# Performance work log

Measured on AMD Instinct MI355X. Metric: run time of the kernel, lower is better.

Reference implementation:

```python
import jax, jax.numpy as jnp
import numpy as np

B, T, E, H, D = 2, 2048, 1024, 16, 64   # batch, seq, n_embd, heads, head_dim
C, P, BF, MH, R, F4 = 64, 64, 256, 128, 8, 4096  # ctx_dim, prototypes, basis, mod hidden, gate rank, 4*n_embd


def _rms(x):
    return x * jax.lax.rsqrt(jnp.mean(x * x, axis=-1, keepdims=True) + 1e-6)


def _rotary(x, cos, sin):
    d = x.shape[-1] // 2
    x1, x2 = x[..., :d], x[..., d:]
    return jnp.concatenate([x1 * cos + x2 * sin, -x1 * sin + x2 * cos], axis=-1)


def _ln(x, g, b):
    mu = jnp.mean(x, axis=-1, keepdims=True)
    v = jnp.mean(jnp.square(x - mu), axis=-1, keepdims=True)
    return (x - mu) * jax.lax.rsqrt(v + 1e-5) * g + b


def _remixed(x, ctx, bw, lg, lb, tm, bias, m1w, m1b, m2w, m2b, ogw, ogb, ogB, ogs):
    # RemixedLinear: basis proj -> LayerNorm -> context sigmoid gate -> template mixing -> low-rank output gate
    h = _ln(x @ bw.T, lg, lb)                                              # [B,T,basis]
    gl = jax.nn.gelu(ctx @ m1w.T + m1b, approximate=False) @ m2w.T + m2b   # basis_modulator MLP
    gate_basis = jax.nn.sigmoid(gl)                                        # gate_temperature = 1.0, dense gate
    gate_out = 1.0 + jnp.tanh(ogs * ((ctx @ ogw.T + ogb) @ ogB))           # low-rank output gate
    return (h * gate_basis) @ tm.T * gate_out + bias


def _forward(x, cos, sin, wq, wk, wv, wo, cb_qw, protos,
             fc_bw, fc_lg, fc_lb, fc_tm, fc_b, fc_m1w, fc_m1b, fc_m2w, fc_m2b, fc_ogw, fc_ogb, fc_ogB, fc_ogs,
             pj_bw, pj_lg, pj_lb, pj_tm, pj_b, pj_m1w, pj_m1b, pj_m2w, pj_m2b, pj_ogw, pj_ogb, pj_ogB, pj_ogs):
    b, t, _ = x.shape
    # --- attention with rotary embeddings ---
    xn = _rms(x)
    q = _rotary((xn @ wq.T).reshape(b, t, H, D), cos, sin)
    k = _rotary((xn @ wk.T).reshape(b, t, H, D), cos, sin)
    v = (xn @ wv.T).reshape(b, t, H, D)
    s = jnp.einsum('bqhd,bkhd->bhqk', q, k) * (D ** -0.5)
    mask = jnp.tril(jnp.ones((t, t), dtype=bool))
    s = jnp.where(mask, s, jnp.finfo(s.dtype).min)
    a = jax.nn.softmax(s, axis=-1)
    attn_out = jnp.einsum('bhqk,bkhd->bqhd', a, v).reshape(b, t, E) @ wo.T
    x = x + attn_out
    # --- ContextBank: soft lookup into prototype vocabulary ---
    xn2 = _rms(x)
    cq = xn2 @ cb_qw.T                                  # [B,T,C]
    w = jax.nn.softmax((cq @ protos.T) * (C ** -0.5), axis=-1)
    ctx = w @ protos                                    # [B,T,C]
    # --- RemixedFeedForward: RemixedLinear -> relu^2 -> RemixedLinear ---
    h = _remixed(xn2, ctx, fc_bw, fc_lg, fc_lb, fc_tm, fc_b, fc_m1w, fc_m1b, fc_m2w, fc_m2b, fc_ogw, fc_ogb, fc_ogB, fc_ogs)
    h = jnp.square(jax.nn.relu(h))
    y = _remixed(h, ctx, pj_bw, pj_lg, pj_lb, pj_tm, pj_b, pj_m1w, pj_m1b, pj_m2w, pj_m2b, pj_ogw, pj_ogb, pj_ogB, pj_ogs)
    return x + y


def setup_inputs():
    key = jax.random.key(0)
    ks = jax.random.split(key, 24)
    g = lambda i, shape, s=0.02: jax.random.normal(ks[i], shape, jnp.float32) * s
    t = jnp.arange(T, dtype=jnp.float32)
    inv = 1.0 / (10000.0 ** (jnp.arange(0, D, 2, dtype=jnp.float32) / D))
    ang = t[:, None] * inv                              # [T, D/2]
    return dict(
        x=jax.random.normal(ks[0], (B, T, E), jnp.float32),
        cos=jnp.cos(ang)[None, :, None, :], sin=jnp.sin(ang)[None, :, None, :],
        wq=g(1, (E, E)), wk=g(2, (E, E)), wv=g(3, (E, E)), wo=g(4, (E, E)),
        cb_qw=g(5, (C, E)), protos=g(6, (P, C)),
        fc_bw=g(7, (BF, E)), fc_lg=jnp.ones((BF,)), fc_lb=jnp.zeros((BF,)),
        fc_tm=g(8, (F4, BF), 0.05), fc_b=jnp.zeros((F4,)),
        fc_m1w=g(9, (MH, C)), fc_m1b=jnp.zeros((MH,)),
        fc_m2w=g(10, (BF, MH)), fc_m2b=jnp.zeros((BF,)),
        fc_ogw=g(11, (R, C)), fc_ogb=jnp.zeros((R,)),
        fc_ogB=g(12, (R, F4)), fc_ogs=jnp.full((1,), 0.1, jnp.float32),
        pj_bw=g(13, (BF, F4)), pj_lg=jnp.ones((BF,)), pj_lb=jnp.zeros((BF,)),
        pj_tm=g(14, (E, BF), 0.05), pj_b=jnp.zeros((E,)),
        pj_m1w=g(15, (MH, C)), pj_m1b=jnp.zeros((MH,)),
        pj_m2w=g(16, (BF, MH)), pj_m2b=jnp.zeros((BF,)),
        pj_ogw=g(17, (R, C)), pj_ogb=jnp.zeros((R,)),
        pj_ogB=g(18, (R, E)), pj_ogs=jnp.full((1,), 0.1, jnp.float32),
    )


def reference(x, cos, sin, wq, wk, wv, wo, cb_qw, protos,
              fc_bw, fc_lg, fc_lb, fc_tm, fc_b, fc_m1w, fc_m1b, fc_m2w, fc_m2b, fc_ogw, fc_ogb, fc_ogB, fc_ogs,
              pj_bw, pj_lg, pj_lb, pj_tm, pj_b, pj_m1w, pj_m1b, pj_m2w, pj_m2b, pj_ogw, pj_ogb, pj_ogB, pj_ogs):
    return _forward(x, cos, sin, wq, wk, wv, wo, cb_qw, protos,
                    fc_bw, fc_lg, fc_lb, fc_tm, fc_b, fc_m1w, fc_m1b, fc_m2w, fc_m2b, fc_ogw, fc_ogb, fc_ogB, fc_ogs,
                    pj_bw, pj_lg, pj_lb, pj_tm, pj_b, pj_m1w, pj_m1b, pj_m2w, pj_m2b, pj_ogw, pj_ogb, pj_ogB, pj_ogs)
```

## Files before the change

### kernel.cpp

```cpp
#include <hip/hip_runtime.h>
#include <hip/hip_bf16.h>

typedef unsigned short u16;
typedef unsigned int u32;
typedef __attribute__((ext_vector_type(8))) short bf16x8;
typedef __attribute__((ext_vector_type(4))) float f32x4;
typedef __attribute__((ext_vector_type(4))) u16 u16x4;

#define DEVFN __device__ __forceinline__

DEVFN u16 f2b(float f) {
  u32 u = __builtin_bit_cast(u32, f);
  return (u16)((u + 0x7FFFu + ((u >> 16) & 1u)) >> 16);
}
DEVFN float b2f(u16 b) { return __builtin_bit_cast(float, (u32)b << 16); }

DEVFN void gll16(const void* g, void* l) {
  __builtin_amdgcn_global_load_lds((const __attribute__((address_space(1))) void*)g,
                                   (__attribute__((address_space(3))) void*)l, 16, 0, 0);
}
#define BARRIER() __builtin_amdgcn_s_barrier()

constexpr int Tc = 2048, Ec = 1024, Hc = 16, Cc = 64, BFc = 256, F4c = 4096;
constexpr int Mc = 2 * Tc;
constexpr float C8 = 0.18033688f;
constexpr float NEG2LOG2E = -2.8853901f;

constexpr size_t MB = 1ull << 20;
constexpr size_t O_XN  = 0;
constexpr size_t O_HBF = 8 * MB;
constexpr size_t O_QB  = 40 * MB;
constexpr size_t O_H1  = 40 * MB;
constexpr size_t O_A2  = 40 * MB;
constexpr size_t O_KB  = 48 * MB;
constexpr size_t O_H2  = 48 * MB;
constexpr size_t O_VBF = 56 * MB;
constexpr size_t O_CQ  = 64 * MB;
constexpr size_t O_GO1 = 68 * MB + 512 * 1024;
constexpr size_t O_GO2 = 68 * MB + 640 * 1024;
constexpr size_t O_GB1 = 69 * MB;
constexpr size_t O_VT  = 72 * MB;
constexpr size_t O_GB2 = 73 * MB;
constexpr size_t O_A1  = 77 * MB;
constexpr size_t O_X2  = 80 * MB;
constexpr size_t O_WQ  = 96 * MB, O_WK = 98 * MB, O_WV = 100 * MB, O_WO = 102 * MB;
constexpr size_t O_CBQ = 104 * MB;
constexpr size_t O_FCBW = O_CBQ + 256 * 1024;
constexpr size_t O_FCTM = 105 * MB;
constexpr size_t O_PJBW = 107 * MB;
constexpr size_t O_PJTM = 109 * MB;

struct Cvt9 {
  const float* s[9];
  u16* d[9];
  int cum[10];
};
__global__ __launch_bounds__(256) void k_cvt(Cvt9 a) {
  int i = blockIdx.x * 256 + threadIdx.x;
  int seg = 0;
  #pragma unroll
  for (int s = 1; s < 9; s++) seg += (i >= a.cum[s]);
  int off = i - a.cum[seg];
  float4 v = *(const float4*)&a.s[seg][(size_t)off * 4];
  u16x4 o; o.x = f2b(v.x); o.y = f2b(v.y); o.z = f2b(v.z); o.w = f2b(v.w);
  *(u16x4*)&a.d[seg][(size_t)off * 4] = o;
}

DEVFN float bsum256(float v, float* sb) {
  #pragma unroll
  for (int off = 32; off; off >>= 1) v += __shfl_down(v, off);
  __syncthreads();
  if ((threadIdx.x & 63) == 0) sb[threadIdx.x >> 6] = v;
  __syncthreads();
  return (sb[0] + sb[1]) + (sb[2] + sb[3]);
}

__global__ __launch_bounds__(256) void k_rms(const float* __restrict__ x, u16* __restrict__ o) {
  __shared__ float sb[4];
  int row = blockIdx.x, tid = threadIdx.x;
  float4 v = *(const float4*)&x[(size_t)row * 1024 + tid * 4];
  float s = bsum256(v.x * v.x + v.y * v.y + v.z * v.z + v.w * v.w, sb);
  float r = rsqrtf(s * (1.f / 1024.f) + 1e-6f);
  u16x4 ov;
  ov.x = f2b(v.x * r); ov.y = f2b(v.y * r); ov.z = f2b(v.z * r); ov.w = f2b(v.w * r);
  *(u16x4*)&o[(size_t)row * 1024 + tid * 4] = ov;
}

__global__ __launch_bounds__(256) void k_vtrans(const u16* __restrict__ vb, u16* __restrict__ vt) {
  __shared__ u16 tl[64][65];
  int t0 = blockIdx.x * 64, bh = blockIdx.y;
  int b = bh >> 4, h = bh & 15, tid = threadIdx.x;
  #pragma unroll
  for (int rep = 0; rep < 16; rep++) {
    int idx = rep * 256 + tid, r = idx >> 6, c = idx & 63;
    tl[r][c] = vb[((size_t)(b * 2048 + t0 + r)) * 1024 + h * 64 + c];
  }
  __syncthreads();
  #pragma unroll
  for (int rep = 0; rep < 16; rep++) {
    int idx = rep * 256 + tid, d = idx >> 6, tt = idx & 63;
    vt[((size_t)bh * 64 + d) * 2048 + t0 + tt] = tl[tt][d];
  }
}

#define MFMA16(A, B, C) __builtin_amdgcn_mfma_f32_16x16x32_bf16(A, B, C, 0, 0, 0)
__global__ __launch_bounds__(256) void k_attn(const u16* __restrict__ Q, const u16* __restrict__ Kb,
                                              const u16* __restrict__ VT, u16* __restrict__ O) {
  const int i = blockIdx.x;
  const int wrk = (i & 7) * 64 + (i >> 3);
  const int hb = wrk >> 4, xp = wrk & 15;
  const int b = hb >> 4, h = hb & 15;
  const int tid = threadIdx.x, lane = tid & 63, w = tid >> 6;
  const int lr = lane & 15, lg = lane >> 4;
  const size_t TE = 2048ull * 1024ull;
  const u16* Qp = Q + (size_t)b * TE + (size_t)h * 64;
  const u16* Kp = Kb + (size_t)b * TE + (size_t)h * 64;
  const u16* Vp = VT + ((size_t)(b * 16 + h)) * 64ull * 2048ull;
  u16* Op = O + (size_t)b * TE + (size_t)h * 64;
  __shared__ __align__(16) u16 Ks[2][4096];
  __shared__ __align__(16) u16 Vs[2][4096];
  __shared__ __align__(16) u16 Ps[4][1024];
  auto stageKV = [&](int j0, int buf) {
    #pragma unroll
    for (int c = 0; c < 2; c++) {
      int u = c * 256 + tid;
      int row = u >> 3, slot = u & 7;
      int cg = slot ^ (row & 7);
      gll16(&Kp[(size_t)(j0 + row) * 1024 + cg * 8], &Ks[buf][u * 8]);
    }
    #pragma unroll
    for (int c = 0; c < 2; c++) {
      int u = c * 256 + tid;
      int row = u >> 3, slot = u & 7;
      int cg = slot ^ (row & 7);
      gll16(&Vp[(size_t)row * 2048 + j0 + cg * 8], &Vs[buf][u * 8]);
    }
  };
  auto run_tile = [&](int qb) {
    const int q0 = qb * 64, qw0 = q0 + w * 16;
    bf16x8 qf0 = *(const bf16x8*)&Qp[(size_t)(qw0 + lr) * 1024 + lg * 8];
    bf16x8 qf1 = *(const bf16x8*)&Qp[(size_t)(qw0 + lr) * 1024 + 32 + lg * 8];
    f32x4 o0 = {}, o1 = {}, o2 = {}, o3 = {};
    float m = -1e30f, l = 0.f;
    const int NT = qb + 1;
    stageKV(0, 0);
    int cur = 0;
    for (int it = 0; it < NT; it++) {
      if (it + 1 < NT) {
        stageKV((it + 1) * 64, cur ^ 1);
        asm volatile("s_waitcnt vmcnt(4)" ::: "memory");
      } else {
        asm volatile("s_waitcnt vmcnt(0)" ::: "memory");
      }
      BARRIER();
      const int j0 = it * 64;
      const u16* Kl = Ks[cur];
      const u16* Vl = Vs[cur];
      f32x4 c4[4];
      __builtin_amdgcn_s_setprio(1);
      #pragma unroll
      for (int kg = 0; kg < 4; kg++) {
        f32x4 cc = {};
        int r = kg * 16 + lr;
        bf16x8 ka0 = *(const bf16x8*)&Kl[r * 64 + ((lg ^ (lr & 7)) * 8)];
        bf16x8 ka1 = *(const bf16x8*)&Kl[r * 64 + (((4 + lg) ^ (lr & 7)) * 8)];
        cc = MFMA16(ka0, qf0, cc);
        cc = MFMA16(ka1, qf1, cc);
        c4[kg] = cc;
      }
      __builtin_amdgcn_s_setprio(0);
      float xs[16];
      #pragma unroll
      for (int kg = 0; kg < 4; kg++)
        #pragma unroll
        for (int r = 0; r < 4; r++) xs[kg * 4 + r] = c4[kg][r];
      if (it == NT - 1) {
        int q = qw0 + lr;
        #pragma unroll
        for (int kg = 0; kg < 4; kg++)
          #pragma unroll
          for (int r = 0; r < 4; r++)
            if (j0 + kg * 16 + lg * 4 + r > q) xs[kg * 4 + r] = -1e30f;
      }
      float tm = xs[0];
      #pragma unroll
      for (int r = 1; r < 16; r++) tm = fmaxf(tm, xs[r]);
      tm = fmaxf(tm, __shfl_xor(tm, 16));
      tm = fmaxf(tm, __shfl_xor(tm, 32));
      if (!__all(tm <= m + 64.f)) {
        float mn = fmaxf(m, tm);
        float al = exp2f((m - mn) * C8);
        m = mn;
        l *= al;
        float ar0 = __shfl(al, lg * 4 + 0), ar1 = __shfl(al, lg * 4 + 1);
        float ar2 = __shfl(al, lg * 4 + 2), ar3 = __shfl(al, lg * 4 + 3);
        o0[0] *= ar0; o0[1] *= ar1; o0[2] *= ar2; o0[3] *= ar3;
        o1[0] *= ar0; o1[1] *= ar1; o1[2] *= ar2; o1[3] *= ar3;
        o2[0] *= ar0; o2[1] *= ar1; o2[2] *= ar2; o2[3] *= ar3;
        o3[0] *= ar0; o3[1] *= ar1; o3[2] *= ar2; o3[3] *= ar3;
      }
      const float mnC = -m * C8;
      float p[16], rs = 0.f;
      #pragma unroll
      for (int r = 0; r < 16; r++) { p[r] = exp2f(fmaf(xs[r], C8, mnC)); rs += p[r]; }
      rs += __shfl_xor(rs, 16);
      rs += __shfl_xor(rs, 32);
      l += rs;
      #pragma unroll
      for (int kg = 0; kg < 4; kg++) {
        int unit = (kg >> 1) * 64 + ((kg & 1) * 2 + (lg >> 1)) * 16 + lr;
        u16x4 pk;
        pk.x = f2b(p[kg * 4 + 0]); pk.y = f2b(p[kg * 4 + 1]);
        pk.z = f2b(p[kg * 4 + 2]); pk.w = f2b(p[kg * 4 + 3]);
        *(u16x4*)&Ps[w][unit * 8 + (lg & 1) * 4] = pk;
      }
      bf16x8 pa0 = *(const bf16x8*)&Ps[w][(lg * 16 + lr) * 8];
      bf16x8 pa1 = *(const bf16x8*)&Ps[w][(64 + lg * 16 + lr) * 8];
      __builtin_amdgcn_s_setprio(1);
      #pragma unroll
      for (int dg = 0; dg < 4; dg++) {
        int dr = dg * 16 + lr;
        bf16x8 v0 = *(const bf16x8*)&Vl[dr * 64 + ((lg ^ (lr & 7)) * 8)];
        bf16x8 v1 = *(const bf16x8*)&Vl[dr * 64 + (((4 + lg) ^ (lr & 7)) * 8)];
        f32x4& od = (dg == 0) ? o0 : (dg == 1) ? o1 : (dg == 2) ? o2 : o3;
        od = MFMA16(pa0, v0, od);
        od = MFMA16(pa1, v1, od);
      }
      __builtin_amdgcn_s_setprio(0);
      BARRIER();
      cur ^= 1;
    }
    float li0 = 1.f / __shfl(l, lg * 4 + 0), li1 = 1.f / __shfl(l, lg * 4 + 1);
    float li2 = 1.f / __shfl(l, lg * 4 + 2), li3 = 1.f / __shfl(l, lg * 4 + 3);
    #pragma unroll
    for (int r = 0; r < 4; r++) {
      float lir = (r == 0) ? li0 : (r == 1) ? li1 : (r == 2) ? li2 : li3;
      size_t ro = (size_t)(qw0 + lg * 4 + r) * 1024;
      Op[ro + lr]      = f2b(o0[r] * lir);
      Op[ro + 16 + lr] = f2b(o1[r] * lir);
      Op[ro + 32 + lr] = f2b(o2[r] * lir);
      Op[ro + 48 + lr] = f2b(o3[r] * lir);
    }
  };
  run_tile(xp);
  run_tile(31 - xp);
}

template <int BM, int BN, int WR, int WC, int EPI>
__global__ __launch_bounds__(256) void gemm_bt(
    const u16* __restrict__ A, const u16* __restrict__ Bw,
    float* __restrict__ Co, u16* __restrict__ Cb, u16* __restrict__ Cb2, u16* __restrict__ Cb3,
    int gM, int N, int K, int KS,
    const float* __restrict__ e0, const float* __restrict__ e1,
    const float* __restrict__ e2, const float* __restrict__ e3,
    const float* __restrict__ e4) {
  constexpr int WM = BM / WR, WN = BN / WC;
  constexpr int FM = WM / 16, FN = WN / 16;
  constexpr int ACH = BM / 64, BCH = BN / 64;
  static_assert(WR * WC == 4 && BM % 64 == 0 && BN % 64 == 0, "cfg");
  __shared__ __align__(16) u16 As[2][BM * 32];
  __shared__ __align__(16) u16 Bs[2][BN * 32];
  const int tid = threadIdx.x;
  const int lane = tid & 63, wid = tid >> 6;
  const int wr = wid / WC, wc = wid % WC;
  const int bm = blockIdx.y * BM, bn = blockIdx.x * BN;
  const int lr = lane & 15, lg = lane >> 4;
  const int arow0 = bm + wr * WM, bcol0 = bn + wc * WN;
  const int kbeg = blockIdx.z * KS, kend = kbeg + KS;
  f32x4 acc[FM][FN] = {};
  auto stage = [&](int k0, int buf) {
    #pragma unroll
    for (int c = 0; c < ACH; c++) {
      int u = c * 256 + tid;
      int row = u >> 2, slot = u & 3;
      int cg = slot ^ (row & 3) ^ ((row >> 2) & 3);
      gll16(&A[(size_t)(bm + row) * K + k0 + cg * 8], &As[buf][u * 8]);
    }
    #pragma unroll
    for (int c = 0; c < BCH; c++) {
      int u = c * 256 + tid;
      int row = u >> 2, slot = u & 3;
      int cg = slot ^ (row & 3) ^ ((row >> 2) & 3);
      gll16(&Bw[(size_t)(bn + row) * K + k0 + cg * 8], &Bs[buf][u * 8]);
    }
  };
  stage(kbeg, 0);
  int cur = 0;
  for (int k0 = kbeg; k0 < kend; k0 += 32) {
    __syncthreads();
    if (k0 + 32 < kend) stage(k0 + 32, cur ^ 1);
    const u16* Ab = As[cur];
    const u16* Bb = Bs[cur];
    bf16x8 af[FM], bfr[FN];
    #pragma unroll
    for (int i = 0; i < FM; i++) {
      int tr = wr * WM + i * 16 + lr;
      af[i] = *(const bf16x8*)&Ab[tr * 32 + ((lg ^ (tr & 3) ^ ((tr >> 2) & 3)) * 8)];
    }
    #pragma unroll
    for (int j = 0; j < FN; j++) {
      int tr = wc * WN + j * 16 + lr;
      bfr[j] = *(const bf16x8*)&Bb[tr * 32 + ((lg ^ (tr & 3) ^ ((tr >> 2) & 3)) * 8)];
    }
    #pragma unroll
    for (int i = 0; i < FM; i++)
      #pragma unroll
      for (int j = 0; j < FN; j++)
        acc[i][j] = __builtin_amdgcn_mfma_f32_16x16x32_bf16(af[i], bfr[j], acc[i][j], 0, 0, 0);
    cur ^= 1;
  }
  const int nb0 = bcol0 + lr;
  if constexpr (EPI == 0 || EPI == 2) {
    float* Cz = Co + (size_t)blockIdx.z * ((size_t)gM * N);
    #pragma unroll
    for (int i = 0; i < FM; i++)
      #pragma unroll
      for (int r = 0; r < 4; r++) {
        size_t mrow = (size_t)(arow0 + i * 16 + lg * 4 + r);
        #pragma unroll
        for (int j = 0; j < FN; j++) {
          float v = acc[i][j][r];
          if constexpr (EPI == 2) v += e4[mrow * N + nb0 + j * 16];
          Cz[mrow * N + nb0 + j * 16] = v;
        }
      }
  } else if constexpr (EPI == 8) {
    if (bn < 2048) {
      u16* dst = (bn < 1024) ? Cb : Cb2;
      const int nq0 = (bcol0 & 1023) + lr;
      #pragma unroll
      for (int i = 0; i < FM; i++)
        #pragma unroll
        for (int r = 0; r < 4; r++) {
          size_t mrow = (size_t)(arow0 + i * 16 + lg * 4 + r);
          int t = (int)(mrow & 2047);
          #pragma unroll
          for (int j = 0; j < 2; j++) {
            int d = lr + j * 16;
            float cth = e0[t * 32 + d], sth = e1[t * 32 + d];
            float x1 = acc[i][j][r], x2 = acc[i][j + 2][r];
            dst[mrow * 1024 + nq0 + j * 16]       = f2b(x1 * cth + x2 * sth);
            dst[mrow * 1024 + nq0 + (j + 2) * 16] = f2b(x2 * cth - x1 * sth);
          }
        }
    } else {
      const int nv0 = (bcol0 - 2048) + lr;
      #pragma unroll
      for (int i = 0; i < FM; i++)
        #pragma unroll
        for (int r = 0; r < 4; r++) {
          size_t mrow = (size_t)(arow0 + i * 16 + lg * 4 + r);
          #pragma unroll
          for (int j = 0; j < FN; j++)
            Cb3[mrow * 1024 + nv0 + j * 16] = f2b(acc[i][j][r]);
        }
    }
  } else if constexpr (EPI == 7) {
    #pragma unroll
    for (int i = 0; i < FM; i++)
      #pragma unroll
      for (int r = 0; r < 4; r++) {
        size_t mrow = (size_t)(arow0 + i * 16 + lg * 4 + r);
        #pragma unroll
        for (int j = 0; j < FN; j++)
          Cb[mrow * N + nb0 + j * 16] = f2b(acc[i][j][r]);
      }
  } else {
    const float cg = e3[0] * NEG2LOG2E;
    float gB[FN][8], bias[FN];
    #pragma unroll
    for (int j = 0; j < FN; j++) {
      int n = nb0 + j * 16;
      bias[j] = e2[n];
      #pragma unroll
      for (int rr = 0; rr < 8; rr++) gB[j][rr] = e1[(size_t)rr * N + n];
    }
    #pragma unroll
    for (int i = 0; i < FM; i++)
      #pragma unroll
      for (int r = 0; r < 4; r++) {
        size_t mrow = (size_t)(arow0 + i * 16 + lg * 4 + r);
        float go8[8];
        #pragma unroll
        for (int rr = 0; rr < 8; rr++) go8[rr] = e0[mrow * 8 + rr];
        #pragma unroll
        for (int j = 0; j < FN; j++) {
          float d = 0.f;
          #pragma unroll
          for (int rr = 0; rr < 8; rr++) d += go8[rr] * gB[j][rr];
          float gate = 2.f * __builtin_amdgcn_rcpf(1.f + exp2f(cg * d));
          float v = acc[i][j][r] * gate + bias[j];
          if constexpr (EPI == 3) {
            v = fmaxf(v, 0.f); v *= v;
            Cb[mrow * N + nb0 + j * 16] = f2b(v);
          } else {
            v += e4[mrow * N + nb0 + j * 16];
            Co[mrow * N + nb0 + j * 16] = v;
          }
        }
      }
  }
}

__global__ __launch_bounds__(256) void k_ctxgate(
    const float* __restrict__ cqp, const float* __restrict__ pr,
    const float* __restrict__ f_m1w, const float* __restrict__ f_m1b,
    const float* __restrict__ f_m2w, const float* __restrict__ f_m2b,
    const float* __restrict__ f_ogw, const float* __restrict__ f_ogb,
    const float* __restrict__ p_m1w, const float* __restrict__ p_m1b,
    const float* __restrict__ p_m2w, const float* __restrict__ p_m2b,
    const float* __restrict__ p_ogw, const float* __restrict__ p_ogb,
    float* __restrict__ gb1, float* __restrict__ go1,
    float* __restrict__ gb2, float* __restrict__ go2) {
  __shared__ float pl[64 * 65];
  __shared__ __align__(16) float cqs[16][64];
  __shared__ float wl[16][64];
  __shared__ __align__(16) float cs[16][64];
  __shared__ __align__(16) float gls[16][128];
  const int tid = threadIdx.x;
  const int row0 = blockIdx.x * 16;
  for (int idx = tid; idx < 4096; idx += 256) pl[(idx >> 6) * 65 + (idx & 63)] = pr[idx];
  for (int idx = tid; idx < 1024; idx += 256) {
    int r = idx >> 6, c = idx & 63;
    float s = 0.f;
    #pragma unroll
    for (int z = 0; z < 4; z++) s += cqp[(size_t)z * Mc * 64 + (size_t)(row0 + r) * 64 + c];
    cqs[r][c] = s;
  }
  __syncthreads();
  const int row = tid >> 4, pg = tid & 15;
  float sc[4];
  #pragma unroll
  for (int q = 0; q < 4; q++) {
    int p = pg * 4 + q;
    float s = 0.f;
    #pragma unroll
    for (int k4 = 0; k4 < 16; k4++) {
      float4 cv = *(const float4*)&cqs[row][k4 * 4];
      const float* pw = &pl[p * 65 + k4 * 4];
      s += cv.x * pw[0] + cv.y * pw[1] + cv.z * pw[2] + cv.w * pw[3];
    }
    sc[q] = s * 0.125f;
  }
  float mx = fmaxf(fmaxf(sc[0], sc[1]), fmaxf(sc[2], sc[3]));
  #pragma unroll
  for (int off = 1; off <= 8; off <<= 1) mx = fmaxf(mx, __shfl_xor(mx, off));
  float e[4], sum = 0.f;
  #pragma unroll
  for (int q = 0; q < 4; q++) { e[q] = __expf(sc[q] - mx); sum += e[q]; }
  #pragma unroll
  for (int off = 1; off <= 8; off <<= 1) sum += __shfl_xor(sum, off);
  float inv = 1.f / sum;
  #pragma unroll
  for (int q = 0; q < 4; q++) wl[row][pg * 4 + q] = e[q] * inv;
  __syncthreads();
  #pragma unroll
  for (int q = 0; q < 4; q++) {
    int c = pg * 4 + q;
    float a = 0.f;
    for (int p = 0; p < 64; p++) a += wl[row][p] * pl[p * 65 + c];
    cs[row][c] = a;
  }
  __syncthreads();
  auto gate = [&](const float* m1w, const float* m1b, const float* m2w, const float* m2b,
                  const float* ogw, const float* ogb, float* gb, float* go) {
    for (int idx = tid; idx < 2048; idx += 256) {
      int r = idx >> 7, mh = idx & 127;
      const float* wrow = &m1w[(size_t)mh * 64];
      float a = m1b[mh];
      #pragma unroll
      for (int k4 = 0; k4 < 16; k4++) {
        float4 w4 = *(const float4*)&wrow[k4 * 4];
        float4 c4v = *(const float4*)&cs[r][k4 * 4];
        a += c4v.x * w4.x + c4v.y * w4.y + c4v.z * w4.z + c4v.w * w4.w;
      }
      gls[r][mh] = 0.5f * a * (1.f + erff(a * 0.70710678f));
    }
    if (tid < 128) {
      int r = tid >> 3, rr = tid & 7;
      const float* wrow = &ogw[(size_t)rr * 64];
      float a = ogb[rr];
      #pragma unroll
      for (int k4 = 0; k4 < 16; k4++) {
        float4 w4 = *(const float4*)&wrow[k4 * 4];
        float4 c4v = *(const float4*)&cs[r][k4 * 4];
        a += c4v.x * w4.x + c4v.y * w4.y + c4v.z * w4.z + c4v.w * w4.w;
      }
      go[(size_t)(row0 + r) * 8 + rr] = a;
    }
    __syncthreads();
    int n = tid;
    float acc2[16];
    #pragma unroll
    for (int r = 0; r < 16; r++) acc2[r] = m2b[n];
    for (int k4 = 0; k4 < 32; k4++) {
      float4 wv = *(const float4*)&m2w[(size_t)n * 128 + k4 * 4];
      #pragma unroll
      for (int r = 0; r < 16; r++) {
        float4 g = *(const float4*)&gls[r][k4 * 4];
        acc2[r] += g.x * wv.x + g.y * wv.y + g.z * wv.z + g.w * wv.w;
      }
    }
    #pragma unroll
    for (int r = 0; r < 16; r++)
      gb[(size_t)(row0 + r) * 256 + n] = 1.f / (1.f + __expf(-acc2[r]));
    __syncthreads();
  };
  gate(f_m1w, f_m1b, f_m2w, f_m2b, f_ogw, f_ogb, gb1, go1);
  gate(p_m1w, p_m1b, p_m2w, p_m2b, p_ogw, p_ogb, gb2, go2);
}

template <int NS>
__global__ __launch_bounds__(256) void k_lnmul(const float* __restrict__ h,
                                               const float* __restrict__ g,
                                               const float* __restrict__ b,
                                               const float* __restrict__ gbm,
                                               u16* __restrict__ o) {
  __shared__ float sb[4];
  int row = blockIdx.x, n = threadIdx.x;
  float x = 0.f;
  #pragma unroll
  for (int z = 0; z < NS; z++) x += h[(size_t)z * Mc * 256 + (size_t)row * 256 + n];
  float mu = bsum256(x, sb) * (1.f / 256.f);
  float d = x - mu;
  float var = bsum256(d * d, sb) * (1.f / 256.f);
  float y = d * rsqrtf(var + 1e-5f) * g[n] + b[n];
  o[(size_t)row * 256 + n] = f2b(y * gbm[(size_t)row * 256 + n]);
}

extern "C" void kernel_launch(void* const* d_in, const int* in_sizes, int n_in,
                              void* d_out, int out_size, void* d_ws, size_t ws_size,
                              hipStream_t stream) {
  (void)in_sizes; (void)n_in; (void)out_size; (void)ws_size;
  const float* x      = (const float*)d_in[0];
  const float* cosb   = (const float*)d_in[1];
  const float* sinb   = (const float*)d_in[2];
  const float* wq     = (const float*)d_in[3];
  const float* wk     = (const float*)d_in[4];
  const float* wv     = (const float*)d_in[5];
  const float* wo     = (const float*)d_in[6];
  const float* cb_qw  = (const float*)d_in[7];
  const float* protos = (const float*)d_in[8];
  const float* fc_bw  = (const float*)d_in[9];
  const float* fc_lg  = (const float*)d_in[10];
  const float* fc_lb  = (const float*)d_in[11];
  const float* fc_tm  = (const float*)d_in[12];
  const float* fc_b   = (const float*)d_in[13];
  const float* fc_m1w = (const float*)d_in[14];
  const float* fc_m1b = (const float*)d_in[15];
  const float* fc_m2w = (const float*)d_in[16];
  const float* fc_m2b = (const float*)d_in[17];
  const float* fc_ogw = (const float*)d_in[18];
  const float* fc_ogb = (const float*)d_in[19];
  const float* fc_ogB = (const float*)d_in[20];
  const float* fc_ogs = (const float*)d_in[21];
  const float* pj_bw  = (const float*)d_in[22];
  const float* pj_lg  = (const float*)d_in[23];
  const float* pj_lb  = (const float*)d_in[24];
  const float* pj_tm  = (const float*)d_in[25];
  const float* pj_b   = (const float*)d_in[26];
  const float* pj_m1w = (const float*)d_in[27];
  const float* pj_m1b = (const float*)d_in[28];
  const float* pj_m2w = (const float*)d_in[29];
  const float* pj_m2b = (const float*)d_in[30];
  const float* pj_ogw = (const float*)d_in[31];
  const float* pj_ogb = (const float*)d_in[32];
  const float* pj_ogB = (const float*)d_in[33];
  const float* pj_ogs = (const float*)d_in[34];
  char* ws = (char*)d_ws;
  float* outp = (float*)d_out;
  auto U = [&](size_t o) { return (u16*)(ws + o); };
  auto F = [&](size_t o) { return (float*)(ws + o); };
  const float* nf = nullptr;
  u16* nu = nullptr;

  {
    Cvt9 a;
    const float* srcs[9] = {wq, wk, wv, wo, cb_qw, fc_bw, fc_tm, pj_bw, pj_tm};
    size_t offs[9] = {O_WQ, O_WK, O_WV, O_WO, O_CBQ, O_FCBW, O_FCTM, O_PJBW, O_PJTM};
    int ns[9] = {Ec*Ec, Ec*Ec, Ec*Ec, Ec*Ec, Cc*Ec, BFc*Ec, F4c*BFc, BFc*F4c, Ec*BFc};
    int cum = 0;
    for (int s = 0; s < 9; s++) {
      a.s[s] = srcs[s]; a.d[s] = U(offs[s]); a.cum[s] = cum; cum += ns[s] / 4;
    }
    a.cum[9] = cum;
    k_cvt<<<dim3(cum / 256), dim3(256), 0, stream>>>(a);
  }
  k_rms<<<dim3(Mc), dim3(256), 0, stream>>>(x, U(O_XN));
  gemm_bt<128,128,2,2,8><<<dim3(24,32), dim3(256), 0, stream>>>(U(O_XN), U(O_WQ), nullptr, U(O_QB), U(O_KB), U(O_VBF), Mc, 3072, Ec, Ec, cosb, sinb, nf, nf, nf);
  k_vtrans<<<dim3(Tc / 64, 2 * Hc), dim3(256), 0, stream>>>(U(O_VBF), U(O_VT));
  k_attn<<<dim3(512), dim3(256), 0, stream>>>(U(O_QB), U(O_KB), U(O_VT), U(O_XN));
  gemm_bt<128,128,2,2,2><<<dim3(8,32), dim3(256), 0, stream>>>(U(O_XN), U(O_WO), F(O_X2), nu, nu, nu, Mc, Ec, Ec, Ec, nf, nf, nf, nf, x);
  k_rms<<<dim3(Mc), dim3(256), 0, stream>>>(F(O_X2), U(O_XN));
  gemm_bt<64,64,1,4,0><<<dim3(1,64,4), dim3(256), 0, stream>>>(U(O_XN), U(O_CBQ), F(O_CQ), nu, nu, nu, Mc, Cc, Ec, 256, nf, nf, nf, nf, nf);
  k_ctxgate<<<dim3(Mc / 16), dim3(256), 0, stream>>>(F(O_CQ), protos,
      fc_m1w, fc_m1b, fc_m2w, fc_m2b, fc_ogw, fc_ogb,
      pj_m1w, pj_m1b, pj_m2w, pj_m2b, pj_ogw, pj_ogb,
      F(O_GB1), F(O_GO1), F(O_GB2), F(O_GO2));
  gemm_bt<64,64,1,4,0><<<dim3(4,64,2), dim3(256), 0, stream>>>(U(O_XN), U(O_FCBW), F(O_H1), nu, nu, nu, Mc, BFc, Ec, 512, nf, nf, nf, nf, nf);
  k_lnmul<2><<<dim3(Mc), dim3(256), 0, stream>>>(F(O_H1), fc_lg, fc_lb, F(O_GB1), U(O_A1));
  gemm_bt<128,128,2,2,3><<<dim3(32,32), dim3(256), 0, stream>>>(U(O_A1), U(O_FCTM), nullptr, U(O_HBF), nu, nu, Mc, F4c, BFc, BFc, F(O_GO1), fc_ogB, fc_b, fc_ogs, nf);
  gemm_bt<64,64,1,4,0><<<dim3(4,64,4), dim3(256), 0, stream>>>(U(O_HBF), U(O_PJBW), F(O_H2), nu, nu, nu, Mc, BFc, F4c, 1024, nf, nf, nf, nf, nf);
  k_lnmul<4><<<dim3(Mc), dim3(256), 0, stream>>>(F(O_H2), pj_lg, pj_lb, F(O_GB2), U(O_A2));
  gemm_bt<128,128,2,2,4><<<dim3(8,32), dim3(256), 0, stream>>>(U(O_A2), U(O_PJTM), outp, nu, nu, nu, Mc, Ec, BFc, BFc, F(O_GO2), pj_ogB, pj_b, pj_ogs, F(O_X2));
}
```

Before: 418.0 us.

## Fuse context-query and fc basis GEMMs, rework GEMM pipeline waits, pack bf16 conversions

The context-bank query GEMM and the fc basis-projection GEMM both read the same normalized activations, so they are merged into one GEMM with N=320 and no split-K. A new epilogue routes the first 64 columns to the context query and the remaining 256 to the basis output, which drops the split-K partial sums and lets k_lnmul run with one partial. The GEMM main loop swaps __syncthreads for explicit vmcnt waits around the prefetch plus barriers. The attention kernel packs P to bf16 with v_cvt_pk_bf16_f32 and unrolls the row-max reduction, and a few scratch buffer offsets move to avoid overlap.

```diff
diff --git a/kernel.cpp b/kernel.cpp
--- a/kernel.cpp
+++ b/kernel.cpp
@@ -14,12 +14,28 @@
   return (u16)((u + 0x7FFFu + ((u >> 16) & 1u)) >> 16);
 }
 DEVFN float b2f(u16 b) { return __builtin_bit_cast(float, (u32)b << 16); }
+DEVFN u32 cvtpk(float lo, float hi) {
+  u32 r;
+  asm("v_cvt_pk_bf16_f32 %0, %1, %2" : "=v"(r) : "v"(lo), "v"(hi));
+  return r;
+}
 
 DEVFN void gll16(const void* g, void* l) {
   __builtin_amdgcn_global_load_lds((const __attribute__((address_space(1))) void*)g,
                                    (__attribute__((address_space(3))) void*)l, 16, 0, 0);
 }
 #define BARRIER() __builtin_amdgcn_s_barrier()
+
+template <int N> DEVFN void waitvm() {
+  if constexpr (N == 0) asm volatile("s_waitcnt vmcnt(0)" ::: "memory");
+  else if constexpr (N == 1) asm volatile("s_waitcnt vmcnt(1)" ::: "memory");
+  else if constexpr (N == 2) asm volatile("s_waitcnt vmcnt(2)" ::: "memory");
+  else if constexpr (N == 3) asm volatile("s_waitcnt vmcnt(3)" ::: "memory");
+  else if constexpr (N == 4) asm volatile("s_waitcnt vmcnt(4)" ::: "memory");
+  else if constexpr (N == 5) asm volatile("s_waitcnt vmcnt(5)" ::: "memory");
+  else if constexpr (N == 6) asm volatile("s_waitcnt vmcnt(6)" ::: "memory");
+  else asm volatile("s_waitcnt vmcnt(8)" ::: "memory");
+}
 
 constexpr int Tc = 2048, Ec = 1024, Hc = 16, Cc = 64, BFc = 256, F4c = 4096;
 constexpr int Mc = 2 * Tc;
@@ -31,7 +47,7 @@
 constexpr size_t O_HBF = 8 * MB;
 constexpr size_t O_QB  = 40 * MB;
 constexpr size_t O_H1  = 40 * MB;
-constexpr size_t O_A2  = 40 * MB;
+constexpr size_t O_A2  = 45 * MB;
 constexpr size_t O_KB  = 48 * MB;
 constexpr size_t O_H2  = 48 * MB;
 constexpr size_t O_VBF = 56 * MB;
@@ -45,7 +61,7 @@
 constexpr size_t O_X2  = 80 * MB;
 constexpr size_t O_WQ  = 96 * MB, O_WK = 98 * MB, O_WV = 100 * MB, O_WO = 102 * MB;
 constexpr size_t O_CBQ = 104 * MB;
-constexpr size_t O_FCBW = O_CBQ + 256 * 1024;
+constexpr size_t O_FCBW = O_CBQ + 128 * 1024;
 constexpr size_t O_FCTM = 105 * MB;
 constexpr size_t O_PJBW = 107 * MB;
 constexpr size_t O_PJTM = 109 * MB;
@@ -148,9 +164,9 @@
     for (int it = 0; it < NT; it++) {
       if (it + 1 < NT) {
         stageKV((it + 1) * 64, cur ^ 1);
-        asm volatile("s_waitcnt vmcnt(4)" ::: "memory");
+        waitvm<4>();
       } else {
-        asm volatile("s_waitcnt vmcnt(0)" ::: "memory");
+        waitvm<0>();
       }
       BARRIER();
       const int j0 = it * 64;
@@ -182,9 +198,14 @@
           for (int r = 0; r < 4; r++)
             if (j0 + kg * 16 + lg * 4 + r > q) xs[kg * 4 + r] = -1e30f;
       }
-      float tm = xs[0];
-      #pragma unroll
-      for (int r = 1; r < 16; r++) tm = fmaxf(tm, xs[r]);
+      float tm = fmaxf(xs[0], xs[1]);
+      tm = fmaxf(fmaxf(tm, xs[2]), xs[3]);
+      tm = fmaxf(fmaxf(tm, xs[4]), xs[5]);
+      tm = fmaxf(fmaxf(tm, xs[6]), xs[7]);
+      tm = fmaxf(fmaxf(tm, xs[8]), xs[9]);
+      tm = fmaxf(fmaxf(tm, xs[10]), xs[11]);
+      tm = fmaxf(fmaxf(tm, xs[12]), xs[13]);
+      tm = fmaxf(fmaxf(tm, xs[14]), xs[15]);
       tm = fmaxf(tm, __shfl_xor(tm, 16));
       tm = fmaxf(tm, __shfl_xor(tm, 32));
       if (!__all(tm <= m + 64.f)) {
@@ -209,10 +230,10 @@
       #pragma unroll
       for (int kg = 0; kg < 4; kg++) {
         int unit = (kg >> 1) * 64 + ((kg & 1) * 2 + (lg >> 1)) * 16 + lr;
-        u16x4 pk;
-        pk.x = f2b(p[kg * 4 + 0]); pk.y = f2b(p[kg * 4 + 1]);
-        pk.z = f2b(p[kg * 4 + 2]); pk.w = f2b(p[kg * 4 + 3]);
-        *(u16x4*)&Ps[w][unit * 8 + (lg & 1) * 4] = pk;
+        uint2 pk;
+        pk.x = cvtpk(p[kg * 4 + 0], p[kg * 4 + 1]);
+        pk.y = cvtpk(p[kg * 4 + 2], p[kg * 4 + 3]);
+        *(uint2*)&Ps[w][unit * 8 + (lg & 1) * 4] = pk;
       }
       bf16x8 pa0 = *(const bf16x8*)&Ps[w][(lg * 16 + lr) * 8];
       bf16x8 pa1 = *(const bf16x8*)&Ps[w][(64 + lg * 16 + lr) * 8];
@@ -287,8 +308,13 @@
   stage(kbeg, 0);
   int cur = 0;
   for (int k0 = kbeg; k0 < kend; k0 += 32) {
-    __syncthreads();
-    if (k0 + 32 < kend) stage(k0 + 32, cur ^ 1);
+    if (k0 + 32 < kend) {
+      stage(k0 + 32, cur ^ 1);
+      waitvm<ACH + BCH>();
+    } else {
+      waitvm<0>();
+    }
+    BARRIER();
     const u16* Ab = As[cur];
     const u16* Bb = Bs[cur];
     bf16x8 af[FM], bfr[FN];
@@ -307,6 +333,7 @@
       #pragma unroll
       for (int j = 0; j < FN; j++)
         acc[i][j] = __builtin_amdgcn_mfma_f32_16x16x32_bf16(af[i], bfr[j], acc[i][j], 0, 0, 0);
+    BARRIER();
     cur ^= 1;
   }
   const int nb0 = bcol0 + lr;
@@ -324,6 +351,30 @@
           Cz[mrow * N + nb0 + j * 16] = v;
         }
       }
+  } else if constexpr (EPI == 9) {
+    if (bn == 0) {
+      #pragma unroll
+      for (int i = 0; i < FM; i++)
+        #pragma unroll
+        for (int r = 0; r < 4; r++) {
+          size_t mrow = (size_t)(arow0 + i * 16 + lg * 4 + r);
+          #pragma unroll
+          for (int j = 0; j < FN; j++)
+            Co[mrow * 64 + nb0 + j * 16] = acc[i][j][r];
+        }
+    } else {
+      float* H = (float*)Cb;
+      const int c0 = bcol0 - 64 + lr;
+      #pragma unroll
+      for (int i = 0; i < FM; i++)
+        #pragma unroll
+        for (int r = 0; r < 4; r++) {
+          size_t mrow = (size_t)(arow0 + i * 16 + lg * 4 + r);
+          #pragma unroll
+          for (int j = 0; j < FN; j++)
+            H[mrow * 256 + c0 + j * 16] = acc[i][j][r];
+        }
+    }
   } else if constexpr (EPI == 8) {
     if (bn < 2048) {
       u16* dst = (bn < 1024) ? Cb : Cb2;
@@ -355,16 +406,6 @@
             Cb3[mrow * 1024 + nv0 + j * 16] = f2b(acc[i][j][r]);
         }
     }
-  } else if constexpr (EPI == 7) {
-    #pragma unroll
-    for (int i = 0; i < FM; i++)
-      #pragma unroll
-      for (int r = 0; r < 4; r++) {
-        size_t mrow = (size_t)(arow0 + i * 16 + lg * 4 + r);
-        #pragma unroll
-        for (int j = 0; j < FN; j++)
-          Cb[mrow * N + nb0 + j * 16] = f2b(acc[i][j][r]);
-      }
   } else {
     const float cg = e3[0] * NEG2LOG2E;
     float gB[FN][8], bias[FN];
@@ -403,7 +444,7 @@
 }
 
 __global__ __launch_bounds__(256) void k_ctxgate(
-    const float* __restrict__ cqp, const float* __restrict__ pr,
+    const float* __restrict__ cq, const float* __restrict__ pr,
     const float* __restrict__ f_m1w, const float* __restrict__ f_m1b,
     const float* __restrict__ f_m2w, const float* __restrict__ f_m2b,
     const float* __restrict__ f_ogw, const float* __restrict__ f_ogb,
@@ -420,13 +461,8 @@
   const int tid = threadIdx.x;
   const int row0 = blockIdx.x * 16;
   for (int idx = tid; idx < 4096; idx += 256) pl[(idx >> 6) * 65 + (idx & 63)] = pr[idx];
-  for (int idx = tid; idx < 1024; idx += 256) {
-    int r = idx >> 6, c = idx & 63;
-    float s = 0.f;
-    #pragma unroll
-    for (int z = 0; z < 4; z++) s += cqp[(size_t)z * Mc * 64 + (size_t)(row0 + r) * 64 + c];
-    cqs[r][c] = s;
-  }
+  for (int idx = tid; idx < 1024; idx += 256)
+    cqs[idx >> 6][idx & 63] = cq[(size_t)row0 * 64 + idx];
   __syncthreads();
   const int row = tid >> 4, pg = tid & 15;
   float sc[4];
@@ -592,13 +628,12 @@
   k_attn<<<dim3(512), dim3(256), 0, stream>>>(U(O_QB), U(O_KB), U(O_VT), U(O_XN));
   gemm_bt<128,128,2,2,2><<<dim3(8,32), dim3(256), 0, stream>>>(U(O_XN), U(O_WO), F(O_X2), nu, nu, nu, Mc, Ec, Ec, Ec, nf, nf, nf, nf, x);
   k_rms<<<dim3(Mc), dim3(256), 0, stream>>>(F(O_X2), U(O_XN));
-  gemm_bt<64,64,1,4,0><<<dim3(1,64,4), dim3(256), 0, stream>>>(U(O_XN), U(O_CBQ), F(O_CQ), nu, nu, nu, Mc, Cc, Ec, 256, nf, nf, nf, nf, nf);
+  gemm_bt<64,64,1,4,9><<<dim3(5,64), dim3(256), 0, stream>>>(U(O_XN), U(O_CBQ), F(O_CQ), (u16*)F(O_H1), nu, nu, Mc, 320, Ec, Ec, nf, nf, nf, nf, nf);
   k_ctxgate<<<dim3(Mc / 16), dim3(256), 0, stream>>>(F(O_CQ), protos,
       fc_m1w, fc_m1b, fc_m2w, fc_m2b, fc_ogw, fc_ogb,
       pj_m1w, pj_m1b, pj_m2w, pj_m2b, pj_ogw, pj_ogb,
       F(O_GB1), F(O_GO1), F(O_GB2), F(O_GO2));
-  gemm_bt<64,64,1,4,0><<<dim3(4,64,2), dim3(256), 0, stream>>>(U(O_XN), U(O_FCBW), F(O_H1), nu, nu, nu, Mc, BFc, Ec, 512, nf, nf, nf, nf, nf);
-  k_lnmul<2><<<dim3(Mc), dim3(256), 0, stream>>>(F(O_H1), fc_lg, fc_lb, F(O_GB1), U(O_A1));
+  k_lnmul<1><<<dim3(Mc), dim3(256), 0, stream>>>(F(O_H1), fc_lg, fc_lb, F(O_GB1), U(O_A1));
   gemm_bt<128,128,2,2,3><<<dim3(32,32), dim3(256), 0, stream>>>(U(O_A1), U(O_FCTM), nullptr, U(O_HBF), nu, nu, Mc, F4c, BFc, BFc, F(O_GO1), fc_ogB, fc_b, fc_ogs, nf);
   gemm_bt<64,64,1,4,0><<<dim3(4,64,4), dim3(256), 0, stream>>>(U(O_HBF), U(O_PJBW), F(O_H2), nu, nu, nu, Mc, BFc, F4c, 1024, nf, nf, nf, nf, nf);
   k_lnmul<4><<<dim3(Mc), dim3(256), 0, stream>>>(F(O_H2), pj_lg, pj_lb, F(O_GB2), U(O_A2));
```

New measurement: 419.0 us. Within noise of the previous version (+0.2%).
